# Performance work log

Measured on AMD Instinct MI355X. Metric: run time of the kernel, lower is better.

Reference implementation:

```python
import jax, jax.numpy as jnp
import numpy as np

NUM_GRAPHS = 64
NUM_EDGE_TYPES = 3


def gat_conv(x, src, dst, W, a_src, a_dst, bias, num_nodes, heads, ch):
    # PyG GATConv, concat=False: mean over heads, attention leaky_relu slope 0.2
    xp = (x @ W).reshape(num_nodes, heads, ch)          # [N,H,C]
    al_s = jnp.einsum('nhc,hc->nh', xp, a_src)           # [N,H]
    al_d = jnp.einsum('nhc,hc->nh', xp, a_dst)
    logits = jax.nn.leaky_relu(al_s[src] + al_d[dst], 0.2)  # [E,H]
    m = jax.ops.segment_max(logits, dst, num_segments=num_nodes)
    e = jnp.exp(logits - m[dst])
    denom = jax.ops.segment_sum(e, dst, num_segments=num_nodes)
    alpha = e / denom[dst]                               # segment softmax over dst
    msg = alpha[:, :, None] * xp[src]                    # [E,H,C]
    out = jax.ops.segment_sum(msg, dst, num_segments=num_nodes)  # [N,H,C]
    return out.mean(axis=1) + bias


def lstm_dir(seq, w_ih, w_hh, b_ih, b_hh):
    # seq: [L,N,C]; PyTorch LSTM cell math
    hh = w_hh.shape[1]
    n = seq.shape[1]
    def step(carry, xt):
        h, c = carry
        g = xt @ w_ih.T + b_ih + h @ w_hh.T + b_hh
        i, f, gg, o = jnp.split(g, 4, axis=-1)
        c = jax.nn.sigmoid(f) * c + jax.nn.sigmoid(i) * jnp.tanh(gg)
        h = jax.nn.sigmoid(o) * jnp.tanh(c)
        return (h, c), h
    init = (jnp.zeros((n, hh), seq.dtype), jnp.zeros((n, hh), seq.dtype))
    _, hs = jax.lax.scan(step, init, seq)
    return hs  # [L,N,hh]


def setup_inputs() -> dict:
    key = jax.random.key(0)
    ks = jax.random.split(key, 24)
    N, E, C, H, P, T = 50000, 600000, 128, 4, 2, NUM_EDGE_TYPES
    HH = (P * C) // 2  # JK biLSTM hidden = 128
    s = 0.05
    src = jax.random.randint(ks[0], (E,), 0, N, dtype=jnp.int32)
    off = jax.random.randint(ks[1], (E,), 1, N, dtype=jnp.int32)
    dst = (src + off) % N  # guaranteed self-loop free
    edge_index = jnp.stack([src, dst], axis=0)  # types are contiguous blocks of E//T
    batch = jnp.sort(jax.random.randint(ks[2], (N,), 0, NUM_GRAPHS, dtype=jnp.int32))
    return {
        'x': jax.random.normal(ks[3], (N, C), jnp.float32),
        'edge_index': edge_index,
        'batch': batch,
        'problem_type': jax.random.uniform(ks[4], (NUM_GRAPHS, 1), jnp.float32),
        'gat_W': jax.random.normal(ks[5], (P, T, C, H * C), jnp.float32) * s,
        'gat_att_src': jax.random.normal(ks[6], (P, T, H, C), jnp.float32) * s,
        'gat_att_dst': jax.random.normal(ks[7], (P, T, H, C), jnp.float32) * s,
        'gat_bias': jnp.zeros((P, T, C), jnp.float32),
        'w_ih_fw': jax.random.normal(ks[8], (4 * HH, C), jnp.float32) * s,
        'w_hh_fw': jax.random.normal(ks[9], (4 * HH, HH), jnp.float32) * s,
        'b_ih_fw': jnp.zeros((4 * HH,), jnp.float32),
        'b_hh_fw': jnp.zeros((4 * HH,), jnp.float32),
        'w_ih_bw': jax.random.normal(ks[10], (4 * HH, C), jnp.float32) * s,
        'w_hh_bw': jax.random.normal(ks[11], (4 * HH, HH), jnp.float32) * s,
        'b_ih_bw': jnp.zeros((4 * HH,), jnp.float32),
        'b_hh_bw': jnp.zeros((4 * HH,), jnp.float32),
        'jk_att_w': jax.random.normal(ks[12], (2 * HH, 1), jnp.float32) * s,
        'jk_att_b': jnp.zeros((1,), jnp.float32),
        'fc1_w': jax.random.normal(ks[13], (C + 1, 80), jnp.float32) * s,
        'fc1_b': jnp.zeros((80,), jnp.float32),
        'fc2_w': jax.random.normal(ks[14], (80, 80), jnp.float32) * s,
        'fc2_b': jnp.zeros((80,), jnp.float32),
        'fc3_w': jax.random.normal(ks[15], (80, 10), jnp.float32) * s,
        'fc3_b': jnp.zeros((10,), jnp.float32),
    }


def reference(x, edge_index, batch, problem_type, gat_W, gat_att_src, gat_att_dst,
              gat_bias, w_ih_fw, w_hh_fw, b_ih_fw, b_hh_fw, w_ih_bw, w_hh_bw,
              b_ih_bw, b_hh_bw, jk_att_w, jk_att_b, fc1_w, fc1_b, fc2_w, fc2_b,
              fc3_w, fc3_b):
    N, C = x.shape
    P, T, H, _ = gat_att_src.shape
    E = edge_index.shape[1]
    Et = E // T  # edge types stored in contiguous blocks
    loop = jnp.arange(N, dtype=edge_index.dtype)
    xs = [x]
    cur = x
    for p in range(P):
        acc = jnp.zeros_like(cur)
        for t in range(T):
            src = jnp.concatenate([edge_index[0, t * Et:(t + 1) * Et], loop])
            dst = jnp.concatenate([edge_index[1, t * Et:(t + 1) * Et], loop])
            out = gat_conv(cur, src, dst, gat_W[p, t], gat_att_src[p, t],
                           gat_att_dst[p, t], gat_bias[p, t], N, H, C)
            acc = acc + jax.nn.leaky_relu(out)  # slope 0.01 (F.leaky_relu default)
        cur = acc / T
        xs.append(cur)
    seq = jnp.stack(xs, axis=0)  # [L,N,C], L=P+1
    hf = lstm_dir(seq, w_ih_fw, w_hh_fw, b_ih_fw, b_hh_fw)
    hb = lstm_dir(seq[::-1], w_ih_bw, w_hh_bw, b_ih_bw, b_hh_bw)[::-1]
    h = jnp.concatenate([hf, hb], axis=-1)  # [L,N,2*HH]
    score = jnp.einsum('lnh,ho->lno', h, jk_att_w)[..., 0] + jk_att_b[0]  # [L,N]
    alpha = jax.nn.softmax(score, axis=0)
    xjk = jnp.einsum('ln,lnc->nc', alpha, seq)  # JK-LSTM weighted sum
    pooled = jax.ops.segment_sum(xjk, batch, num_segments=NUM_GRAPHS)  # collate='sum'
    z = jnp.concatenate([pooled, problem_type], axis=1)
    z = jax.nn.leaky_relu(z @ fc1_w + fc1_b)
    z = jax.nn.leaky_relu(z @ fc2_w + fc2_b)
    return z @ fc3_w + fc3_b
```

## Files before the change

kernel.cpp:

```cpp
#include <hip/hip_runtime.h>
#include <cfloat>


typedef __attribute__((ext_vector_type(8))) short short8;
typedef __attribute__((ext_vector_type(4))) float f32x4;

#define DEG_CAP 31

__device__ __forceinline__ float lrelu(float x, float s) { return x > 0.f ? x : s * x; }

__device__ __forceinline__ float sigmf(float x) {
    return __builtin_amdgcn_rcpf(1.f + __expf(-x));
}
__device__ __forceinline__ float tanhf_fast(float x) {
    x = fminf(fmaxf(x, -15.f), 15.f);
    float e = __expf(2.f * x);
    return (e - 1.f) * __builtin_amdgcn_rcpf(e + 1.f);
}

__device__ __forceinline__ unsigned f2bf(float f) {
    unsigned u = __float_as_uint(f);
    return (u + 0x7FFFu + ((u >> 16) & 1u)) >> 16;
}
__device__ __forceinline__ float bf2f(ushort u) {
    return __uint_as_float(((unsigned)u) << 16);
}
__device__ __forceinline__ float bflo(unsigned u) {
    return __uint_as_float(u << 16);
}
__device__ __forceinline__ float bfhi(unsigned u) {
    return __uint_as_float(u & 0xFFFF0000u);
}

__device__ __forceinline__ int xcd_tile(int bid, int nwg) {
    int q = nwg >> 3, r = nwg & 7;
    int xcd = bid & 7, idx = bid >> 3;
    return (xcd < r ? xcd * (q + 1) : r * (q + 1) + (xcd - r) * q) + idx;
}

__device__ __forceinline__ void stage_a_glds(
    char* ldsA, const ushort* __restrict__ A, int row0, int M, int tid)
{
    int wv = tid >> 6, lane = tid & 63;
#pragma unroll
    for (int it = 0; it < 4; ++it) {
        int chunk = it * 8 + wv;
        int d = chunk * 1024 + lane * 16;
        int r = d >> 8;
        int col = (d & 255) ^ ((r & 7) << 4);
        int row = min(row0 + r, M - 1);
        const char* src = (const char*)A + (long)row * 256 + col;
        __builtin_amdgcn_global_load_lds(
            (const __attribute__((address_space(1))) void*)src,
            (__attribute__((address_space(3))) void*)(ldsA + chunk * 1024),
            16, 0, 0);
    }
}
__device__ __forceinline__ void stage_b_glds(
    char* ldsB, const ushort* __restrict__ B, int tid)
{
    int wv = tid >> 6, lane = tid & 63;
#pragma unroll
    for (int it = 0; it < 4; ++it) {
        int chunk = it * 8 + wv;
        int d = chunk * 1024 + lane * 16;
        int r = d >> 8;
        int col = (d & 255) ^ ((r & 7) << 4);
        const char* src = (const char*)B + (long)r * 256 + col;
        __builtin_amdgcn_global_load_lds(
            (const __attribute__((address_space(1))) void*)src,
            (__attribute__((address_space(3))) void*)(ldsB + chunk * 1024),
            16, 0, 0);
    }
}

__device__ __forceinline__ void compute_tile(
    const char* ldsA, const char* ldsB, f32x4 acc[2][4],
    int wr, int wc, int lr, int lk)
{
#pragma unroll
    for (int ks = 0; ks < 4; ++ks) {
        int kb = ks * 64 + lk;
        short8 af[2], bfr[4];
#pragma unroll
        for (int i = 0; i < 2; ++i) {
            int r = wr + i * 16 + lr;
            af[i] = *(const short8*)(ldsA + ((r * 256 + kb) ^ ((r & 7) << 4)));
        }
#pragma unroll
        for (int j = 0; j < 4; ++j) {
            int c = wc + j * 16 + lr;
            bfr[j] = *(const short8*)(ldsB + ((c * 256 + kb) ^ ((c & 7) << 4)));
        }
#pragma unroll
        for (int i = 0; i < 2; ++i)
#pragma unroll
            for (int j = 0; j < 4; ++j)
                acc[i][j] = __builtin_amdgcn_mfma_f32_16x16x32_bf16(af[i], bfr[j], acc[i][j], 0, 0, 0);
    }
}

__global__ __launch_bounds__(512, 4) void gemm_att(
    const ushort* __restrict__ A16, const ushort* __restrict__ Bt,
    ushort* __restrict__ C16, const float* __restrict__ a_s,
    const float* __restrict__ a_d, float* __restrict__ als,
    float* __restrict__ ald, int M, int nwg)
{
    __shared__ char lds[65536];
    __shared__ float smS[128], smD[128];
    char* ldsA = lds;
    char* ldsB = lds + 32768;
    const int tid = threadIdx.x;
    int tile = xcd_tile(blockIdx.x, nwg);
    int row0 = (tile >> 2) * 128;
    int h = tile & 3;
    int col0 = h * 128;
    if (tid < 128) { smS[tid] = 0.f; smD[tid] = 0.f; }
    stage_a_glds(ldsA, A16, row0, M, tid);
    stage_b_glds(ldsB, Bt + (long)col0 * 128, tid);
    __syncthreads();

    const int wv = tid >> 6, lane = tid & 63;
    const int wr = (wv & 3) * 32, wc = (wv >> 2) * 64;
    const int lr = lane & 15;
    const int lk = (lane >> 4) << 4;
    f32x4 acc[2][4] = {};
    compute_tile(ldsA, ldsB, acc, wr, wc, lr, lk);

    const float* asl = a_s + h * 128;
    const float* adl = a_d + h * 128;
#pragma unroll
    for (int i = 0; i < 2; ++i) {
#pragma unroll
        for (int q = 0; q < 4; ++q) {
            float ps = 0.f, pd = 0.f;
            int row = row0 + wr + i * 16 + (lane >> 4) * 4 + q;
#pragma unroll
            for (int j = 0; j < 4; ++j) {
                int cc = wc + j * 16 + lr;
                float v = acc[i][j][q];
                ps += v * asl[cc];
                pd += v * adl[cc];
                if (row < M) C16[(long)row * 512 + col0 + cc] = (ushort)f2bf(v);
            }
#pragma unroll
            for (int off = 8; off; off >>= 1) {
                ps += __shfl_xor(ps, off);
                pd += __shfl_xor(pd, off);
            }
            if (lr == 0) {
                int rl = wr + i * 16 + (lane >> 4) * 4 + q;
                atomicAdd(&smS[rl], ps);
                atomicAdd(&smD[rl], pd);
            }
        }
    }
    __syncthreads();
    if (tid < 128) {
        int row = row0 + tid;
        if (row < M) {
            als[(long)row * 4 + h] = smS[tid];
            ald[(long)row * 4 + h] = smD[tid];
        }
    }
}

__global__ __launch_bounds__(512, 4) void lstm_both(
    const ushort* __restrict__ xb, const ushort* __restrict__ lwt,
    ushort* __restrict__ hbase, ushort* __restrict__ cbase,
    const float* __restrict__ bihf, const float* __restrict__ bhhf,
    const float* __restrict__ bihb, const float* __restrict__ bhhb,
    const float* __restrict__ jkw, float* __restrict__ score,
    int N, int nwg, int jstep)
{
    __shared__ char lds[65536];
    __shared__ float ssc[128];
    char* ldsA = lds;
    char* ldsB = lds + 32768;
    const int tid = threadIdx.x;
    const int dir = blockIdx.y;
    int tile = xcd_tile(blockIdx.x, nwg);
    int row0 = (tile >> 2) * 128;
    int cc = tile & 3;
    if (tid < 128) ssc[tid] = 0.f;

    const int l = dir ? (2 - jstep) : jstep;
    const int first = (jstep == 0), last = (jstep == 2);
    const ushort* Ab = xb + (long)l * N * 128;
    const ushort* Bih = lwt + (long)dir * 2 * 65536;
    const ushort* Bhh = Bih + 65536;
    const ushort* hprev = hbase + (long)((dir << 1) | ((jstep + 1) & 1)) * N * 128;
    ushort* hcur = hbase + (long)((dir << 1) | (jstep & 1)) * N * 128;
    ushort* cbuf = cbase + (long)dir * N * 128;
    const float* bi = dir ? bihb : bihf;
    const float* bh = dir ? bhhb : bhhf;
    const float* jw = jkw + (dir ? 128 : 0);
    float* sc = score + (long)l * N;

    const int wv = tid >> 6, lane = tid & 63;
    const int wr = (wv & 3) * 32, wc = (wv >> 2) * 64;
    const int lr = lane & 15, lg = lane >> 4;
    const int lk = lg << 4;
    f32x4 acc[2][4] = {};

    stage_a_glds(ldsA, Ab, row0, N, tid);
    stage_b_glds(ldsB, Bih + (long)cc * 128 * 128, tid);
    __syncthreads();
    compute_tile(ldsA, ldsB, acc, wr, wc, lr, lk);
    if (!first) {
        __syncthreads();
        stage_a_glds(ldsA, hprev, row0, N, tid);
        stage_b_glds(ldsB, Bhh + (long)cc * 128 * 128, tid);
        __syncthreads();
        compute_tile(ldsA, ldsB, acc, wr, wc, lr, lk);
    }

    const int ch = cc * 32 + (wc >> 6) * 16 + lr;
    const float bI = bi[ch] + bh[ch];
    const float bF = bi[128 + ch] + bh[128 + ch];
    const float bG = bi[256 + ch] + bh[256 + ch];
    const float bO = bi[384 + ch] + bh[384 + ch];
    const float jv = jw[ch];
    float psum[8];
#pragma unroll
    for (int i = 0; i < 2; ++i) {
#pragma unroll
        for (int q = 0; q < 4; ++q) {
            int u = i * 4 + q;
            int row = row0 + wr + i * 16 + lg * 4 + q;
            float p = 0.f;
            if (row < N) {
                long off = (long)row * 128 + ch;
                float cprev = first ? 0.f : bf2f(cbuf[off]);
                float cv = sigmf(acc[i][1][q] + bF) * cprev
                         + sigmf(acc[i][0][q] + bI) * tanhf_fast(acc[i][2][q] + bG);
                float hv = sigmf(acc[i][3][q] + bO) * tanhf_fast(cv);
                if (!last) {
                    cbuf[off] = (ushort)f2bf(cv);
                    hcur[off] = (ushort)f2bf(hv);
                }
                p = hv * jv;
            }
            psum[u] = p;
        }
    }
#pragma unroll
    for (int u = 0; u < 8; ++u) {
        float p = psum[u];
#pragma unroll
        for (int off = 8; off; off >>= 1) p += __shfl_xor(p, off);
        if (lr == 0)
            atomicAdd(&ssc[wr + (u >> 2) * 16 + lg * 4 + (u & 3)], p);
    }
    __syncthreads();
    if (tid < 128) {
        int row = row0 + tid;
        if (row < N) unsafeAtomicAdd(&sc[row], ssc[tid]);
    }
}

__global__ void pack_gatw(const float* __restrict__ gw, ushort* __restrict__ out) {
    int i = blockIdx.x * 256 + threadIdx.x;
    if (i >= 6 * 65536) return;
    int pt = i >> 16, rem = i & 65535, n = rem >> 7, k = rem & 127;
    out[i] = (ushort)f2bf(gw[pt * 65536 + k * 512 + n]);
}
__global__ void pack_lstm(const float* __restrict__ a, const float* __restrict__ b,
                          const float* __restrict__ c, const float* __restrict__ d,
                          ushort* __restrict__ out) {
    int i = blockIdx.x * 256 + threadIdx.x;
    if (i >= 4 * 65536) return;
    const float* p = (i < 65536) ? a : (i < 131072) ? b : (i < 196608) ? c : d;
    int rem = i & 65535;
    int cp = rem >> 7, k = rem & 127;
    int g = (cp >> 4) & 3;
    int ch = ((cp >> 6) << 4) | (cp & 15);
    out[i] = (ushort)f2bf(p[(g * 128 + ch) * 128 + k]);
}
__global__ void pack_x(const float* __restrict__ x, ushort* __restrict__ o, long n) {
    long i = ((long)blockIdx.x * 256 + threadIdx.x) * 4;
    if (i >= n) return;
    float4 v = *(const float4*)(x + i);
    ushort4 u;
    u.x = (ushort)f2bf(v.x); u.y = (ushort)f2bf(v.y);
    u.z = (ushort)f2bf(v.z); u.w = (ushort)f2bf(v.w);
    *(ushort4*)(o + i) = u;
}

__global__ __launch_bounds__(256) void build_csr(
    const int* __restrict__ srcs, const int* __restrict__ dsts,
    int E, int Et, int N, int* __restrict__ cnt, int* __restrict__ bucket)
{
    int i = blockIdx.x * 256 + threadIdx.x;
    if (i >= E) return;
    int t = i / Et;
    int s = srcs[i];
    int d = dsts[i];
    int slot = atomicAdd(&cnt[t * N + d], 1);
    if (slot < DEG_CAP) bucket[((long)(t * N + d)) * DEG_CAP + slot] = s;
}

__global__ __launch_bounds__(256) void gat_gather(
    const int* __restrict__ cnt, const int* __restrict__ bucket,
    const float* __restrict__ als, const float* __restrict__ ald,
    const ushort* __restrict__ xp16, const float* __restrict__ bias,
    float* __restrict__ dstb, ushort* __restrict__ out16, int N, int t, int first)
{
    int lane = threadIdx.x & 63;
    int half = lane >> 5, hl = lane & 31;
    int d = blockIdx.x * 8 + (threadIdx.x >> 6) * 2 + half;
    if (d >= N) d = N - 1;
    int deg = min(cnt[t * N + d], DEG_CAP);
    int s = d;
    if (hl < deg) s = bucket[((long)(t * N + d)) * DEG_CAP + hl];
    bool act = (hl <= deg);
    float4 ad = *(const float4*)(ald + (long)d * 4);
    float l0 = -FLT_MAX, l1 = -FLT_MAX, l2 = -FLT_MAX, l3 = -FLT_MAX;
    if (act) {
        float4 as = *(const float4*)(als + (long)s * 4);
        l0 = lrelu(as.x + ad.x, 0.2f);
        l1 = lrelu(as.y + ad.y, 0.2f);
        l2 = lrelu(as.z + ad.z, 0.2f);
        l3 = lrelu(as.w + ad.w, 0.2f);
    }
    float m0 = l0, m1 = l1, m2 = l2, m3 = l3;
#pragma unroll
    for (int off = 16; off; off >>= 1) {
        m0 = fmaxf(m0, __shfl_xor(m0, off));
        m1 = fmaxf(m1, __shfl_xor(m1, off));
        m2 = fmaxf(m2, __shfl_xor(m2, off));
        m3 = fmaxf(m3, __shfl_xor(m3, off));
    }
    float e0 = 0.f, e1 = 0.f, e2 = 0.f, e3 = 0.f;
    if (act) {
        e0 = __expf(l0 - m0); e1 = __expf(l1 - m1);
        e2 = __expf(l2 - m2); e3 = __expf(l3 - m3);
    }
    float s0 = e0, s1 = e1, s2 = e2, s3 = e3;
#pragma unroll
    for (int off = 16; off; off >>= 1) {
        s0 += __shfl_xor(s0, off);
        s1 += __shfl_xor(s1, off);
        s2 += __shfl_xor(s2, off);
        s3 += __shfl_xor(s3, off);
    }
    float a0 = 0.25f * e0 / s0, a1 = 0.25f * e1 / s1;
    float a2 = 0.25f * e2 / s2, a3 = 0.25f * e3 / s3;

    int md = deg;
#pragma unroll
    for (int off = 32; off; off >>= 1) md = max(md, __shfl_xor(md, off));

    int base = (lane & 32);
    float accL[2] = {0.f, 0.f}, accH[2] = {0.f, 0.f};
    int sj = __shfl(s, base);
    const uint* xs = (const uint*)(xp16 + (long)sj * 512);
    uint c0 = xs[hl], c1 = xs[32 + hl], c2 = xs[64 + hl], c3 = xs[96 + hl];
    uint c4 = xs[128 + hl], c5 = xs[160 + hl], c6 = xs[192 + hl], c7 = xs[224 + hl];
    for (int j = 0; j < md; ++j) {
        int sn = __shfl(s, base + j + 1);
        const uint* xn = (const uint*)(xp16 + (long)sn * 512);
        uint n0 = xn[hl], n1 = xn[32 + hl], n2 = xn[64 + hl], n3 = xn[96 + hl];
        uint n4 = xn[128 + hl], n5 = xn[160 + hl], n6 = xn[192 + hl], n7 = xn[224 + hl];
        float w0 = __shfl(a0, base + j), w1 = __shfl(a1, base + j);
        float w2 = __shfl(a2, base + j), w3 = __shfl(a3, base + j);
        accL[0] += w0 * bflo(c0) + w1 * bflo(c2) + w2 * bflo(c4) + w3 * bflo(c6);
        accH[0] += w0 * bfhi(c0) + w1 * bfhi(c2) + w2 * bfhi(c4) + w3 * bfhi(c6);
        accL[1] += w0 * bflo(c1) + w1 * bflo(c3) + w2 * bflo(c5) + w3 * bflo(c7);
        accH[1] += w0 * bfhi(c1) + w1 * bfhi(c3) + w2 * bfhi(c5) + w3 * bfhi(c7);
        c0 = n0; c1 = n1; c2 = n2; c3 = n3;
        c4 = n4; c5 = n5; c6 = n6; c7 = n7;
    }
    {
        float w0 = __shfl(a0, base + md), w1 = __shfl(a1, base + md);
        float w2 = __shfl(a2, base + md), w3 = __shfl(a3, base + md);
        accL[0] += w0 * bflo(c0) + w1 * bflo(c2) + w2 * bflo(c4) + w3 * bflo(c6);
        accH[0] += w0 * bfhi(c0) + w1 * bfhi(c2) + w2 * bfhi(c4) + w3 * bfhi(c6);
        accL[1] += w0 * bflo(c1) + w1 * bflo(c3) + w2 * bflo(c5) + w3 * bflo(c7);
        accH[1] += w0 * bfhi(c1) + w1 * bfhi(c3) + w2 * bfhi(c5) + w3 * bfhi(c7);
    }

    int chA = 2 * hl;
    int chB = 64 + 2 * hl;
    float r0 = lrelu(accL[0] + bias[chA], 0.01f) * (1.f / 3.f);
    float r1 = lrelu(accH[0] + bias[chA + 1], 0.01f) * (1.f / 3.f);
    float r2 = lrelu(accL[1] + bias[chB], 0.01f) * (1.f / 3.f);
    float r3 = lrelu(accH[1] + bias[chB + 1], 0.01f) * (1.f / 3.f);
    float2* apA = (float2*)(dstb + (long)d * 128) + hl;
    float2* apB = (float2*)(dstb + (long)d * 128 + 64) + hl;
    float2 fA, fB;
    if (first) { fA.x = r0; fA.y = r1; fB.x = r2; fB.y = r3; }
    else {
        float2 pA = *apA, pB = *apB;
        fA.x = pA.x + r0; fA.y = pA.y + r1;
        fB.x = pB.x + r2; fB.y = pB.y + r3;
    }
    *apA = fA; *apB = fB;
    if (out16) {
        ushort2 uA, uB;
        uA.x = (ushort)f2bf(fA.x); uA.y = (ushort)f2bf(fA.y);
        uB.x = (ushort)f2bf(fB.x); uB.y = (ushort)f2bf(fB.y);
        *((ushort2*)(out16 + (long)d * 128) + hl) = uA;
        *((ushort2*)(out16 + (long)d * 128 + 64) + hl) = uB;
    }
}

__global__ void init_z0(const float* __restrict__ ptype, float* __restrict__ z0) {
    int i = blockIdx.x * 128 + threadIdx.x;
    if (i < 64 * 129) z0[i] = ((i % 129) == 128) ? ptype[i / 129] : 0.f;
}

__global__ __launch_bounds__(128) void pool_jk(
    const float* __restrict__ score, const float* __restrict__ x0,
    const float* __restrict__ x1, const float* __restrict__ x2,
    const int* __restrict__ batch, float* __restrict__ z0, int N)
{
    int c = threadIdx.x;
    int n0 = blockIdx.x * 64;
    if (n0 >= N) return;
    int n1 = min(n0 + 64, N);
    float s = 0.f;
    int g = batch[n0];
    for (int n = n0; n < n1; ++n) {
        int b = batch[n];
        if (b != g) { unsafeAtomicAdd(&z0[g * 129 + c], s); s = 0.f; g = b; }
        float s0 = score[n], s1 = score[N + n], s2 = score[2L * N + n];
        float m = fmaxf(s0, fmaxf(s1, s2));
        float e0 = __expf(s0 - m), e1 = __expf(s1 - m), e2 = __expf(s2 - m);
        float inv = __builtin_amdgcn_rcpf(e0 + e1 + e2);
        long i = (long)n * 128 + c;
        s += (e0 * x0[i] + e1 * x1[i] + e2 * x2[i]) * inv;
    }
    unsafeAtomicAdd(&z0[g * 129 + c], s);
}

__global__ __launch_bounds__(128) void mlp_kernel(
    const float* __restrict__ z0, const float* __restrict__ w1, const float* __restrict__ b1,
    const float* __restrict__ w2, const float* __restrict__ b2,
    const float* __restrict__ w3, const float* __restrict__ b3,
    float* __restrict__ out)
{
    int gidx = blockIdx.x, tid = threadIdx.x;
    __shared__ float zin[129], z1[80], z2[80];
    zin[tid] = z0[gidx * 129 + tid];
    if (tid == 0) zin[128] = z0[gidx * 129 + 128];
    __syncthreads();
    if (tid < 80) {
        float s = b1[tid];
        for (int k = 0; k < 129; ++k) s += zin[k] * w1[k * 80 + tid];
        z1[tid] = lrelu(s, 0.01f);
    }
    __syncthreads();
    if (tid < 80) {
        float s = b2[tid];
        for (int k = 0; k < 80; ++k) s += z1[k] * w2[k * 80 + tid];
        z2[tid] = lrelu(s, 0.01f);
    }
    __syncthreads();
    if (tid < 10) {
        float s = b3[tid];
        for (int k = 0; k < 80; ++k) s += z2[k] * w3[k * 10 + tid];
        out[gidx * 10 + tid] = s;
    }
}

extern "C" void kernel_launch(void* const* d_in, const int* in_sizes, int n_in,
                              void* d_out, int out_size, void* d_ws, size_t ws_size,
                              hipStream_t stream)
{
    (void)n_in; (void)out_size; (void)ws_size;
    const float* x      = (const float*)d_in[0];
    const int*   ei     = (const int*)d_in[1];
    const int*   batch  = (const int*)d_in[2];
    const float* ptype  = (const float*)d_in[3];
    const float* gatW   = (const float*)d_in[4];
    const float* gatAs  = (const float*)d_in[5];
    const float* gatAd  = (const float*)d_in[6];
    const float* gatB   = (const float*)d_in[7];
    const float* w_ih_fw = (const float*)d_in[8];
    const float* w_hh_fw = (const float*)d_in[9];
    const float* b_ih_fw = (const float*)d_in[10];
    const float* b_hh_fw = (const float*)d_in[11];
    const float* w_ih_bw = (const float*)d_in[12];
    const float* w_hh_bw = (const float*)d_in[13];
    const float* b_ih_bw = (const float*)d_in[14];
    const float* b_hh_bw = (const float*)d_in[15];
    const float* jkw    = (const float*)d_in[16];
    const float* fc1w   = (const float*)d_in[18];
    const float* fc1b   = (const float*)d_in[19];
    const float* fc2w   = (const float*)d_in[20];
    const float* fc2b   = (const float*)d_in[21];
    const float* fc3w   = (const float*)d_in[22];
    const float* fc3b   = (const float*)d_in[23];

    const int N = in_sizes[0] / 128;
    const int E = in_sizes[1] / 2;
    const int Et = E / 3;
    const long NC = (long)N * 128;

    float* w = (float*)d_ws;
    float* xp   = w; w += (long)N * 512;
    float* l1   = w; w += NC;
    float* l2   = w; w += NC;
    float* accb = w; w += NC;
    float* outm = w; w += NC;
    ushort* xb16 = (ushort*)w; w += 3L * N * 64;
    float* als  = w; w += (long)N * 4;
    float* ald  = w; w += (long)N * 4;
    float* score = w; w += 3L * N;
    ushort* gwt = (ushort*)w; w += 6 * 65536 / 2;
    ushort* lwt = (ushort*)w; w += 4 * 65536 / 2;
    float* z0   = w; w += 64 * 129 + 4;

    int* cnt    = (int*)outm;
    int* bucket = cnt + 3L * N;
    ushort* xp16 = (ushort*)xp;
    ushort* hbase = xp16 + (long)N * 512;
    ushort* cbase = (ushort*)outm;

    pack_gatw<<<(6 * 65536 + 255) / 256, 256, 0, stream>>>(gatW, gwt);
    pack_lstm<<<(4 * 65536 + 255) / 256, 256, 0, stream>>>(w_ih_fw, w_hh_fw, w_ih_bw, w_hh_bw, lwt);
    pack_x<<<(int)((NC / 4 + 255) / 256), 256, 0, stream>>>(x, xb16, NC);
    hipMemsetAsync(score, 0, sizeof(float) * 3 * N, stream);
    hipMemsetAsync(cnt, 0, sizeof(int) * 3 * N, stream);
    build_csr<<<(E + 255) / 256, 256, 0, stream>>>(ei, ei + E, E, Et, N, cnt, bucket);

    const int RB = (N + 127) / 128;
    const int nwg = RB * 4;

    for (int p = 0; p < 2; ++p) {
        const ushort* curA = xb16 + (long)p * N * 128;
        float* dstb = (p == 0) ? l1 : l2;
        ushort* d16 = xb16 + (long)(p + 1) * N * 128;
        for (int t = 0; t < 3; ++t) {
            int pt = p * 3 + t;
            gemm_att<<<nwg, 512, 0, stream>>>(curA, gwt + (long)pt * 65536, xp16,
                                              gatAs + pt * 512, gatAd + pt * 512,
                                              als, ald, N, nwg);
            gat_gather<<<(N + 7) / 8, 256, 0, stream>>>(cnt, bucket, als, ald, xp16,
                                                        gatB + pt * 128, dstb,
                                                        (t == 2) ? d16 : nullptr,
                                                        N, t, t == 0);
        }
    }

    for (int j = 0; j < 3; ++j) {
        lstm_both<<<dim3(nwg, 2), 512, 0, stream>>>(
            xb16, lwt, hbase, cbase, b_ih_fw, b_hh_fw, b_ih_bw, b_hh_bw,
            jkw, score, N, nwg, j);
    }

    init_z0<<<65, 128, 0, stream>>>(ptype, z0);
    pool_jk<<<(N + 63) / 64, 128, 0, stream>>>(score, x, l1, l2, batch, z0, N);
    mlp_kernel<<<64, 128, 0, stream>>>(z0, fc1w, fc1b, fc2w, fc2b, fc3w, fc3b,
                                       (float*)d_out);
}
```

Measured before the change: 723.5 us.

## Double-buffer LSTM input and hidden tiles in LDS, drop init_z0 kernel

The LSTM kernel now issues global-to-LDS loads for both the input tile and the recurrent hidden-state tile into separate 64KB LDS regions up front. It waits with partial vmcnt counts so the second tile's loads overlap the first tile's MFMA compute, which removes one barrier round-trip. Doubling LDS to 128KB drops occupancy from 4 to 2 workgroups per CU. Separately, the init_z0 kernel is replaced by a memset, with problem_type read directly in the MLP kernel, saving one launch.

```diff
diff --git a/kernel.cpp b/kernel.cpp
--- a/kernel.cpp
+++ b/kernel.cpp
@@ -165,7 +165,7 @@
     }
 }
 
-__global__ __launch_bounds__(512, 4) void lstm_both(
+__global__ __launch_bounds__(512, 2) void lstm_both(
     const ushort* __restrict__ xb, const ushort* __restrict__ lwt,
     ushort* __restrict__ hbase, ushort* __restrict__ cbase,
     const float* __restrict__ bihf, const float* __restrict__ bhhf,
@@ -173,10 +173,12 @@
     const float* __restrict__ jkw, float* __restrict__ score,
     int N, int nwg, int jstep)
 {
-    __shared__ char lds[65536];
+    __shared__ char lds[131072];
     __shared__ float ssc[128];
-    char* ldsA = lds;
-    char* ldsB = lds + 32768;
+    char* ldsA1 = lds;
+    char* ldsB1 = lds + 32768;
+    char* ldsA2 = lds + 65536;
+    char* ldsB2 = lds + 98304;
     const int tid = threadIdx.x;
     const int dir = blockIdx.y;
     int tile = xcd_tile(blockIdx.x, nwg);
@@ -203,16 +205,23 @@
     const int lk = lg << 4;
     f32x4 acc[2][4] = {};
 
-    stage_a_glds(ldsA, Ab, row0, N, tid);
-    stage_b_glds(ldsB, Bih + (long)cc * 128 * 128, tid);
-    __syncthreads();
-    compute_tile(ldsA, ldsB, acc, wr, wc, lr, lk);
+    stage_a_glds(ldsA1, Ab, row0, N, tid);
+    stage_b_glds(ldsB1, Bih + (long)cc * 128 * 128, tid);
     if (!first) {
-        __syncthreads();
-        stage_a_glds(ldsA, hprev, row0, N, tid);
-        stage_b_glds(ldsB, Bhh + (long)cc * 128 * 128, tid);
-        __syncthreads();
-        compute_tile(ldsA, ldsB, acc, wr, wc, lr, lk);
+        stage_a_glds(ldsA2, hprev, row0, N, tid);
+        stage_b_glds(ldsB2, Bhh + (long)cc * 128 * 128, tid);
+        asm volatile("s_waitcnt vmcnt(8)" ::: "memory");
+    } else {
+        asm volatile("s_waitcnt vmcnt(0)" ::: "memory");
+    }
+    __builtin_amdgcn_s_barrier();
+    __builtin_amdgcn_sched_barrier(0);
+    compute_tile(ldsA1, ldsB1, acc, wr, wc, lr, lk);
+    if (!first) {
+        asm volatile("s_waitcnt vmcnt(0)" ::: "memory");
+        __builtin_amdgcn_s_barrier();
+        __builtin_amdgcn_sched_barrier(0);
+        compute_tile(ldsA2, ldsB2, acc, wr, wc, lr, lk);
     }
 
     const int ch = cc * 32 + (wc >> 6) * 16 + lr;
@@ -405,11 +414,6 @@
     }
 }
 
-__global__ void init_z0(const float* __restrict__ ptype, float* __restrict__ z0) {
-    int i = blockIdx.x * 128 + threadIdx.x;
-    if (i < 64 * 129) z0[i] = ((i % 129) == 128) ? ptype[i / 129] : 0.f;
-}
-
 __global__ __launch_bounds__(128) void pool_jk(
     const float* __restrict__ score, const float* __restrict__ x0,
     const float* __restrict__ x1, const float* __restrict__ x2,
@@ -423,7 +427,7 @@
     int g = batch[n0];
     for (int n = n0; n < n1; ++n) {
         int b = batch[n];
-        if (b != g) { unsafeAtomicAdd(&z0[g * 129 + c], s); s = 0.f; g = b; }
+        if (b != g) { unsafeAtomicAdd(&z0[g * 128 + c], s); s = 0.f; g = b; }
         float s0 = score[n], s1 = score[N + n], s2 = score[2L * N + n];
         float m = fmaxf(s0, fmaxf(s1, s2));
         float e0 = __expf(s0 - m), e1 = __expf(s1 - m), e2 = __expf(s2 - m);
@@ -431,19 +435,20 @@
         long i = (long)n * 128 + c;
         s += (e0 * x0[i] + e1 * x1[i] + e2 * x2[i]) * inv;
     }
-    unsafeAtomicAdd(&z0[g * 129 + c], s);
+    unsafeAtomicAdd(&z0[g * 128 + c], s);
 }
 
 __global__ __launch_bounds__(128) void mlp_kernel(
-    const float* __restrict__ z0, const float* __restrict__ w1, const float* __restrict__ b1,
+    const float* __restrict__ z0, const float* __restrict__ ptype,
+    const float* __restrict__ w1, const float* __restrict__ b1,
     const float* __restrict__ w2, const float* __restrict__ b2,
     const float* __restrict__ w3, const float* __restrict__ b3,
     float* __restrict__ out)
 {
     int gidx = blockIdx.x, tid = threadIdx.x;
     __shared__ float zin[129], z1[80], z2[80];
-    zin[tid] = z0[gidx * 129 + tid];
-    if (tid == 0) zin[128] = z0[gidx * 129 + 128];
+    zin[tid] = z0[gidx * 128 + tid];
+    if (tid == 0) zin[128] = ptype[gidx];
     __syncthreads();
     if (tid < 80) {
         float s = b1[tid];
@@ -510,7 +515,7 @@
     float* score = w; w += 3L * N;
     ushort* gwt = (ushort*)w; w += 6 * 65536 / 2;
     ushort* lwt = (ushort*)w; w += 4 * 65536 / 2;
-    float* z0   = w; w += 64 * 129 + 4;
+    float* z0   = w; w += 64 * 128 + 4;
 
     int* cnt    = (int*)outm;
     int* bucket = cnt + 3L * N;
@@ -523,6 +528,7 @@
     pack_x<<<(int)((NC / 4 + 255) / 256), 256, 0, stream>>>(x, xb16, NC);
     hipMemsetAsync(score, 0, sizeof(float) * 3 * N, stream);
     hipMemsetAsync(cnt, 0, sizeof(int) * 3 * N, stream);
+    hipMemsetAsync(z0, 0, sizeof(float) * 64 * 128, stream);
     build_csr<<<(E + 255) / 256, 256, 0, stream>>>(ei, ei + E, E, Et, N, cnt, bucket);
 
     const int RB = (N + 127) / 128;
@@ -550,8 +556,7 @@
             jkw, score, N, nwg, j);
     }
 
-    init_z0<<<65, 128, 0, stream>>>(ptype, z0);
     pool_jk<<<(N + 63) / 64, 128, 0, stream>>>(score, x, l1, l2, batch, z0, N);
-    mlp_kernel<<<64, 128, 0, stream>>>(z0, fc1w, fc1b, fc2w, fc2b, fc3w, fc3b,
-                                       (float*)d_out);
-}
+    mlp_kernel<<<64, 128, 0, stream>>>(z0, ptype, fc1w, fc1b, fc2w, fc2b,
+                                       fc3w, fc3b, (float*)d_out);
+}
```

Measured after the change: 844.0 us. +16.7%, slower.
